# Optimization experiments

Hardware: AMD Instinct MI355X
Metric: run time of the kernel (lower is better)

The kernel has to match this reference:

```python
import jax, jax.numpy as jnp
import numpy as np

SIZE = 128
WIN = SIZE // 4   # sliding-window size == region size (32)
HALF = WIN // 2   # 16


def _conv(x, w, pad, groups=1):
    return jax.lax.conv_general_dilated(x, w, (1, 1), [(pad, pad), (pad, pad)],
        dimension_numbers=('NCHW', 'OIHW', 'NCHW'), feature_group_count=groups)


def _resize(x, h, w):
    # F.interpolate(..., mode='bilinear', align_corners=False)
    return jax.image.resize(x, (x.shape[0], x.shape[1], h, w), 'bilinear', antialias=False)


def _gauss_kernels():
    ax = np.linspace(-2.0, 2.0, 5)
    xx, yy = np.meshgrid(ax, ax)
    g = np.exp(-(xx ** 2 + yy ** 2) / 2.0) / (2.0 * np.pi)  # sigma = 1
    gx = (-xx * g).astype(np.float32)
    gy = (-yy * g).astype(np.float32)
    return (jnp.asarray(np.tile(gx[None, None], (3, 3, 1, 1))),
            jnp.asarray(np.tile(gy[None, None], (3, 3, 1, 1))))


def _edge_extract(x):
    Gx, Gy = _gauss_kernels()
    h = _conv(x, Gx, 2)
    v = _conv(x, Gy, 2)
    return jnp.tanh(jnp.sqrt(h * h + v * v + 1e-8))


def _color_moments(x, win=5):
    # F.unfold-based local mean / unbiased var / skewness, via depthwise box sums
    C = x.shape[1]
    n = float(win * win)
    ones = jnp.ones((C, 1, win, win), x.dtype)
    box = lambda z: _conv(z, ones, win // 2, groups=C)
    s1 = box(x); s2 = box(x * x); s3 = box(x * x * x)
    mean = s1 / n
    var = (s2 - n * mean * mean) / (n - 1.0)               # unbiased, matches torch.var
    m3 = (s3 - 3.0 * mean * s2 + 2.0 * n * mean ** 3) / n  # E[(x-m)^3]
    skew = m3 / (jnp.sqrt(jnp.maximum(var, 0.0)) ** 3 + 1e-6)
    return jnp.concatenate([mean, var, skew], 1)


def _locate_region(c):
    # scipy: gradient magnitude < 0.2 -> 4-connected label at argmax -> bbox center
    H, W = c.shape
    flat = jnp.argmax(c)
    xm = (flat // W).astype(jnp.int32)
    ym = (flat % W).astype(jnp.int32)
    gm = jnp.hypot(jnp.gradient(c, axis=0), jnp.gradient(c, axis=1))
    mask = gm < 0.2
    seed = jnp.zeros((H, W), bool).at[xm, ym].set(True) & mask

    def dil(r):
        d = r
        d = d | jnp.pad(r[1:, :], ((0, 1), (0, 0)))
        d = d | jnp.pad(r[:-1, :], ((1, 0), (0, 0)))
        d = d | jnp.pad(r[:, 1:], ((0, 0), (0, 1)))
        d = d | jnp.pad(r[:, :-1], ((0, 0), (1, 0)))
        return d & mask

    def body(s):
        r, _ = s
        nr = dil(r)
        return (nr, jnp.any(nr != r))

    region, _ = jax.lax.while_loop(lambda s: s[1], body, (seed, jnp.any(seed)))
    rows = jnp.any(region, 1); cols = jnp.any(region, 0)
    rs = jnp.argmax(rows); re = H - jnp.argmax(rows[::-1])
    cs = jnp.argmax(cols); ce = W - jnp.argmax(cols[::-1])
    ok = mask[xm, ym]  # label_at_max != 0
    x1 = jnp.where(ok, ((rs + re) // 2).astype(jnp.int32), xm)
    y1 = jnp.where(ok, ((cs + ce) // 2).astype(jnp.int32), ym)
    return x1, y1


def _affine_grid(move, H, W):
    # theta = [[1,0,tx],[0,1,ty]] with (tx,ty)=move, align_corners=False
    bx = (2.0 * jnp.arange(W, dtype=jnp.float32) + 1.0) / W - 1.0
    by = (2.0 * jnp.arange(H, dtype=jnp.float32) + 1.0) / H - 1.0
    gx = bx[None, None, :] + move[:, 0, None, None]
    gy = by[None, :, None] + move[:, 1, None, None]
    return jnp.stack(jnp.broadcast_arrays(gx, gy), -1)  # [B,H,W,2]


def _grid_sample(x, grid):
    # bilinear, zeros padding, align_corners=False (torch defaults)
    B, C, H, W = x.shape
    ix = ((grid[..., 0] + 1.0) * W - 1.0) / 2.0
    iy = ((grid[..., 1] + 1.0) * H - 1.0) / 2.0
    ix0 = jnp.floor(ix).astype(jnp.int32)
    iy0 = jnp.floor(iy).astype(jnp.int32)
    wx1 = ix - ix0; wy1 = iy - iy0
    b = jnp.arange(B)[:, None, None]

    def g(yy, xx):
        valid = ((xx >= 0) & (xx < W) & (yy >= 0) & (yy < H)).astype(x.dtype)
        v = x[b, :, jnp.clip(yy, 0, H - 1), jnp.clip(xx, 0, W - 1)]  # [B,Hg,Wg,C]
        return v * valid[..., None]

    out = (g(iy0, ix0) * ((1 - wy1) * (1 - wx1))[..., None]
         + g(iy0, ix0 + 1) * ((1 - wy1) * wx1)[..., None]
         + g(iy0 + 1, ix0) * (wy1 * (1 - wx1))[..., None]
         + g(iy0 + 1, ix0 + 1) * (wy1 * wx1)[..., None])
    return jnp.transpose(out, (0, 3, 1, 2))


def _bn_relu6(x, w, b):
    # BatchNorm2d in training mode (batch stats, biased var, eps=1e-5) + ReLU6
    m = x.mean((0, 2, 3), keepdims=True)
    v = ((x - m) ** 2).mean((0, 2, 3), keepdims=True)
    y = (x - m) / jnp.sqrt(v + 1e-5) * w[None, :, None, None] + b[None, :, None, None]
    return jnp.clip(y, 0.0, 6.0)


def setup_inputs():
    key = jax.random.key(0)
    ks = jax.random.split(key, 8)
    B, C = 8, 64
    return dict(
        warm_flag=1,
        feat1=jax.random.normal(ks[0], (B, C, SIZE, SIZE), jnp.float32),
        feat2=jax.random.normal(ks[1], (B, C, SIZE, SIZE), jnp.float32),
        cam1=jax.random.uniform(ks[2], (B, 64, 64), jnp.float32),
        cam2=jax.random.uniform(ks[3], (B, 64, 64), jnp.float32),
        f_g=jax.random.uniform(ks[4], (B, 3, 512, 512), jnp.float32),
        f_e=jax.random.uniform(ks[5], (B, 3, 512, 512), jnp.float32),
        conv1_w=jax.random.normal(ks[6], (C, 3, 3, 3), jnp.float32) * 0.1,
        conv1_b=jnp.zeros((C,), jnp.float32),
        conv2_w=jax.random.normal(ks[7], (C, 9, 3, 3), jnp.float32) * 0.1,
        conv2_b=jnp.zeros((C,), jnp.float32),
        bn_w=jnp.ones((C,), jnp.float32),
        bn_b=jnp.zeros((C,), jnp.float32),
    )


def reference(warm_flag, feat1, feat2, cam1, cam2, f_g, f_e,
              conv1_w, conv1_b, conv2_w, conv2_b, bn_w, bn_b):
    B = cam1.shape[0]
    c1 = _resize(cam1[:, None], SIZE, SIZE)
    c2 = _resize(cam2[:, None], SIZE, SIZE)

    if warm_flag == 1:
        # numpy/scipy path in torch is detached from autograd
        c1s = jax.lax.stop_gradient(c1)
        c2s = jax.lax.stop_gradient(c2)
        x1, y1 = jax.vmap(_locate_region)(c1s[:, 0])
        # valid-mode box convolution of cam2 with ones((H//4, W//4)), argmax
        box = jax.lax.conv_general_dilated(c2s, jnp.ones((1, 1, WIN, WIN), c2.dtype), (1, 1),
            'VALID', dimension_numbers=('NCHW', 'OIHW', 'NCHW'))[:, 0]
        Wv = box.shape[-1]
        flat = jnp.argmax(box.reshape(B, -1), -1)
        x2 = (flat // Wv + HALF).astype(jnp.int32)
        y2 = (flat % Wv + HALF).astype(jnp.int32)

        idx = jnp.arange(SIZE)
        def rect(xc, yc):
            r = (idx[None, :] >= jnp.maximum(xc - HALF, 0)[:, None]) & \
                (idx[None, :] < jnp.minimum(xc + HALF, SIZE)[:, None])
            cc = (idx[None, :] >= jnp.maximum(yc - HALF, 0)[:, None]) & \
                 (idx[None, :] < jnp.minimum(yc + HALF, SIZE)[:, None])
            return r[:, None, :, None] & cc[:, None, None, :]
        mask1 = rect(x1, y1).astype(feat1.dtype)
        mask2 = rect(x2, y2).astype(feat2.dtype)
        mi1 = jnp.stack([x1, y1], -1).astype(jnp.float32)
        mi2 = jnp.stack([x2, y2], -1).astype(jnp.float32)
    else:
        mask1 = jnp.zeros_like(feat1)
        mask2 = jnp.zeros_like(feat2)
        mi1 = jnp.zeros((B, 2), jnp.float32)
        mi2 = jnp.zeros((B, 2), jnp.float32)

    cam2_move = (mi2 - mi1) / (SIZE // 2)
    cam1_move = (mi1 - mi2) / (SIZE // 2)
    grid1 = _affine_grid(cam1_move, SIZE, SIZE)
    grid2 = _affine_grid(cam2_move, SIZE, SIZE)

    moments = _resize(_color_moments(f_e), SIZE, SIZE)   # [B,9,128,128]
    edge = _resize(_edge_extract(f_g), SIZE, SIZE)       # [B,3,128,128]
    feat1_edge = jnp.clip(_conv(edge, conv1_w, 1) + conv1_b[None, :, None, None], 0.0, 6.0)
    feat2_color = _conv(moments, conv2_w, 1) + conv2_b[None, :, None, None]

    feat2_move = _grid_sample(feat2_color * mask2, grid2)
    feat1_edge_move = _grid_sample(feat1_edge * mask1, grid1)

    Bc, C, H, W = feat1.shape
    f1 = feat1.reshape(Bc, C, -1)
    f2 = feat2.reshape(Bc, C, -1)
    f2m = feat2_move.reshape(Bc, C, -1)
    f1m = feat1_edge_move.reshape(Bc, C, -1)

    f2_attn = jax.nn.softmax(jnp.einsum('bcn,bdn->bcd', f2m, f1), -1)  # [B,C,C]
    feat1_apply = jnp.einsum('bcd,bdn->bcn', f2_attn, f1).reshape(Bc, C, H, W)
    f1_attn = jax.nn.softmax(jnp.einsum('bcn,bdn->bcd', f1m, f2), -1)
    feat2_apply = jnp.einsum('bcd,bdn->bcn', f1_attn, f2).reshape(Bc, C, H, W)

    feat1_apply = _bn_relu6(feat1_apply, bn_w, bn_b)
    feat2_apply = _bn_relu6(feat2_apply, bn_w, bn_b)

    if warm_flag == 0:
        return (feat1, feat2, grid1, grid2, feat1_edge, feat2_color, f1_attn, f2_attn, feat1, feat2)
    return (feat1_apply, feat2_apply, grid1, grid2, feat1_edge, feat2_color, f1_attn, f2_attn, feat1, feat2)
```

## Files before the change

### kernel.cpp

```cpp
#include <hip/hip_runtime.h>
#include <math.h>

#define SIZE 128
#define WIN 32
#define HALF 16
#define B 8
#define C 64
#define N (SIZE*SIZE)
#define BCN 8388608
#define BV 97

#define O_APPLY1   0
#define O_APPLY2   8388608
#define O_GRID1    16777216
#define O_GRID2    17039360
#define O_EDGEF    17301504
#define O_COLORF   25690112
#define O_ATTN1    34078720
#define O_ATTN2    34111488
#define O_FEAT1    34144256
#define O_FEAT2    42532864

#define WS_BNP     0
#define WS_XY      361472
#define WS_MOM     361600
#define WS_EDGE    1541248
#define WS_BN      1737856

#define NEGINF (-3.402823466e+38f)

typedef unsigned __int128 u128;

__device__ __forceinline__ u128 hfill(u128 g, u128 m) {
  u128 p = m;
  g |= p & (g << 1);  p &= p << 1;
  g |= p & (g << 2);  p &= p << 2;
  g |= p & (g << 4);  p &= p << 4;
  g |= p & (g << 8);  p &= p << 8;
  g |= p & (g << 16); p &= p << 16;
  g |= p & (g << 32); p &= p << 32;
  g |= p & (g << 64);
  p = m;
  g |= p & (g >> 1);  p &= p >> 1;
  g |= p & (g >> 2);  p &= p >> 2;
  g |= p & (g >> 4);  p &= p >> 4;
  g |= p & (g >> 8);  p &= p >> 8;
  g |= p & (g >> 16); p &= p >> 16;
  g |= p & (g >> 32); p &= p >> 32;
  g |= p & (g >> 64);
  return g;
}

__device__ __forceinline__ float resamp(const float* raw, int i, int j) {
  float fy = fminf(fmaxf(0.5f * (float)i - 0.25f, 0.f), 63.f);
  float fx = fminf(fmaxf(0.5f * (float)j - 0.25f, 0.f), 63.f);
  int y0 = (int)fy; float ty = fy - (float)y0; int y1i = min(y0 + 1, 63);
  int x0 = (int)fx; float tx = fx - (float)x0; int x1i = min(x0 + 1, 63);
  float a00 = raw[y0 * 64 + x0],  a01 = raw[y0 * 64 + x1i];
  float a10 = raw[y1i * 64 + x0], a11 = raw[y1i * 64 + x1i];
  return (1.f - ty) * ((1.f - tx) * a00 + tx * a01)
       + ty * ((1.f - tx) * a10 + tx * a11);
}

#define FRONT_B   8
#define PREP_BASE 16
#define COPY_BASE 2064
#define COPY_HALF 8192
#define STAGE1_GRID (COPY_BASE + 2 * COPY_HALF)

__global__ __launch_bounds__(256) void k_stage1(
    const float* __restrict__ cam1, const float* __restrict__ cam2,
    int* __restrict__ xy,
    const float* __restrict__ fe, const float* __restrict__ fg,
    float* __restrict__ mom, float* __restrict__ edge,
    const float4* __restrict__ f1, float4* __restrict__ o8,
    const float4* __restrict__ f2, float4* __restrict__ o9) {
  __shared__ __align__(16) float smem[33824];
  int blk = blockIdx.x;
  int tid = threadIdx.x;

  if (blk >= COPY_BASE) {
    int c = blk - COPY_BASE;
    if (c < COPY_HALF) o8[c * 256 + tid] = f1[c * 256 + tid];
    else { int i = (c - COPY_HALF) * 256 + tid; o9[i] = f2[i]; }
    return;
  }

  if (blk >= PREP_BASE) {
    float* sx = smem;
    int pblk = blk - PREP_BASE;
    if (pblk < 1536) {
      int tile = pblk & 63, ch = (pblk >> 6) % 3, b = pblk / 192;
      int ti0 = (tile >> 3) * 16, tj0 = (tile & 7) * 16;
      const float* src = fe + (size_t)(b * 3 + ch) * 262144;
      int oy0 = 4 * ti0 - 1, ox0 = 4 * tj0 - 1;
      for (int l = tid; l < 66 * 66; l += 256) {
        int r = l / 66, cc = l % 66;
        int gy = oy0 + r, gx = ox0 + cc;
        sx[l] = (gy >= 0 && gy < 512 && gx >= 0 && gx < 512) ? src[gy * 512 + gx] : 0.f;
      }
      __syncthreads();
      int ii = tid >> 4, jj = tid & 15;
      int i = ti0 + ii, j = tj0 + jj;
      float s1a[6], s2a[6], s3a[6], s1b[6], s2b[6], s3b[6];
      #pragma unroll
      for (int t = 0; t < 6; ++t) {
        float a1 = 0, a2 = 0, a3 = 0, b1 = 0, b2 = 0, b3 = 0;
        int lx = 4 * jj + t;
        #pragma unroll
        for (int r = 0; r < 6; ++r) {
          float v = sx[(4 * ii + r) * 66 + lx];
          float v2 = v * v, v3 = v2 * v;
          if (r < 5) { a1 += v; a2 += v2; a3 += v3; }
          if (r > 0) { b1 += v; b2 += v2; b3 += v3; }
        }
        s1a[t] = a1; s2a[t] = a2; s3a[t] = a3;
        s1b[t] = b1; s2b[t] = b2; s3b[t] = b3;
      }
      float am = 0, av = 0, as = 0;
      #pragma unroll
      for (int py = 0; py < 2; ++py) {
        #pragma unroll
        for (int px = 0; px < 2; ++px) {
          float s1 = 0, s2 = 0, s3 = 0;
          #pragma unroll
          for (int t = 0; t < 5; ++t) {
            s1 += py ? s1b[px + t] : s1a[px + t];
            s2 += py ? s2b[px + t] : s2a[px + t];
            s3 += py ? s3b[px + t] : s3a[px + t];
          }
          float mean = s1 / 25.f;
          float var  = (s2 - 25.f * mean * mean) / 24.f;
          float m3   = (s3 - 3.f * mean * s2 + 50.f * mean * mean * mean) / 25.f;
          float sq   = sqrtf(fmaxf(var, 0.f));
          float skew = m3 / (sq * sq * sq + 1e-6f);
          am += mean; av += var; as += skew;
        }
      }
      int base = (b * 9 + ch) * N + i * 128 + j;
      mom[base]         = 0.25f * am;
      mom[base + 3 * N] = 0.25f * av;
      mom[base + 6 * N] = 0.25f * as;
    } else {
      int eblk = pblk - 1536;
      int tile = eblk & 63, b = eblk >> 6;
      int ti0 = (tile >> 3) * 16, tj0 = (tile & 7) * 16;
      const float* s0 = fg + (size_t)b * 3 * 262144;
      int oy0 = 4 * ti0 - 1, ox0 = 4 * tj0 - 1;
      for (int l = tid; l < 66 * 66; l += 256) {
        int r = l / 66, cc = l % 66;
        int gy = oy0 + r, gx = ox0 + cc;
        float v = 0.f;
        if (gy >= 0 && gy < 512 && gx >= 0 && gx < 512) {
          int o = gy * 512 + gx;
          v = s0[o] + s0[262144 + o] + s0[524288 + o];
        }
        sx[l] = v;
      }
      __syncthreads();
      int ii = tid >> 4, jj = tid & 15;
      int i = ti0 + ii, j = tj0 + jj;
      const float INV2PI = 0.15915494309189535f;
      float wg[5], ug[5];
      #pragma unroll
      for (int t = 0; t < 5; ++t) {
        float a = (float)t - 2.f;
        float e = expf(-0.5f * a * a);
        wg[t] = e; ug[t] = -a * e;
      }
      float rAa[6], rAb[6], rBa[6], rBb[6];
      #pragma unroll
      for (int t = 0; t < 6; ++t) {
        float aa = 0, ab = 0, ba = 0, bb = 0;
        int lx = 4 * jj + t;
        #pragma unroll
        for (int r = 0; r < 6; ++r) {
          float v = sx[(4 * ii + r) * 66 + lx];
          if (r < 5) { aa += v * wg[r]; ba += v * ug[r]; }
          if (r > 0) { ab += v * wg[r - 1]; bb += v * ug[r - 1]; }
        }
        rAa[t] = aa; rAb[t] = ab; rBa[t] = ba; rBb[t] = bb;
      }
      float acc = 0.f;
      #pragma unroll
      for (int py = 0; py < 2; ++py) {
        #pragma unroll
        for (int px = 0; px < 2; ++px) {
          float h = 0, v = 0;
          #pragma unroll
          for (int t = 0; t < 5; ++t) {
            float A  = py ? rAb[px + t] : rAa[px + t];
            float Bw = py ? rBb[px + t] : rBa[px + t];
            h += A * ug[t];
            v += Bw * wg[t];
          }
          h *= INV2PI; v *= INV2PI;
          acc += tanhf(sqrtf(h * h + v * v + 1e-8f));
        }
      }
      edge[b * N + i * 128 + j] = 0.25f * acc;
    }
    return;
  }

  if (blk >= FRONT_B) {
    int b = blk - FRONT_B;
    float* raw = smem;
    float* sc2 = smem + 4096;
    float* cs  = smem + 20480;
    float* sv  = smem + 32896;
    int*   si  = (int*)(smem + 33152);

    const float4* c4 = (const float4*)(cam2 + b * 4096);
    float4* r4 = (float4*)raw;
    #pragma unroll
    for (int k = 0; k < 4; ++k) r4[k * 256 + tid] = c4[k * 256 + tid];
    __syncthreads();
    for (int k = 0; k < 64; ++k) {
      int pix = k * 256 + tid;
      sc2[pix] = resamp(raw, pix >> 7, pix & 127);
    }
    __syncthreads();

    for (int idx = tid; idx < BV * 128; idx += 256) {
      int rr = idx >> 7, cc = idx & 127;
      float acc = 0.f;
      #pragma unroll
      for (int dy = 0; dy < WIN; ++dy) acc += sc2[(rr + dy) * 128 + cc];
      cs[idx] = acc;
    }
    __syncthreads();

    float bv = NEGINF; int bi = 0;
    for (int p = tid; p < BV * BV; p += 256) {
      int rr = p / BV, cc = p % BV;
      float s = 0.f;
      #pragma unroll
      for (int dx = 0; dx < WIN; ++dx) s += cs[rr * 128 + cc + dx];
      if (s > bv) { bv = s; bi = p; }
    }
    sv[tid] = bv; si[tid] = bi;
    __syncthreads();
    for (int s = 128; s; s >>= 1) {
      if (tid < s) {
        float ov = sv[tid + s]; int oi = si[tid + s];
        if (ov > sv[tid] || (ov == sv[tid] && oi < si[tid])) { sv[tid] = ov; si[tid] = oi; }
      }
      __syncthreads();
    }
    if (tid == 0) {
      xy[16 + b] = si[0] / BV + HALF;
      xy[24 + b] = si[0] % BV + HALF;
    }
    return;
  }

  {
    int b = blk;
    float* raw = smem;
    float* sc  = smem + 4096;
    float* sv  = smem + 20480;
    int*   si  = (int*)(smem + 20736);
    unsigned long long* mask64 = (unsigned long long*)(smem + 20992);
    int* sint = (int*)(smem + 21504);

    const float4* c4 = (const float4*)(cam1 + b * 4096);
    float4* r4 = (float4*)raw;
    #pragma unroll
    for (int k = 0; k < 4; ++k) r4[k * 256 + tid] = c4[k * 256 + tid];
    __syncthreads();

    float bv = NEGINF; int bi = 0;
    for (int k = 0; k < 64; ++k) {
      int pix = k * 256 + tid;
      float v1 = resamp(raw, pix >> 7, pix & 127);
      sc[pix] = v1;
      if (v1 > bv) { bv = v1; bi = pix; }
    }
    sv[tid] = bv; si[tid] = bi;
    __syncthreads();
    for (int s = 128; s; s >>= 1) {
      if (tid < s) {
        float ov = sv[tid + s]; int oi = si[tid + s];
        if (ov > sv[tid] || (ov == sv[tid] && oi < si[tid])) { sv[tid] = ov; si[tid] = oi; }
      }
      __syncthreads();
    }
    if (tid == 0) { sint[0] = si[0] >> 7; sint[1] = si[0] & 127; }
    __syncthreads();
    int s_xm = sint[0], s_ym = sint[1];

    for (int k = 0; k < 64; ++k) {
      int pix = k * 256 + tid;
      int i = pix >> 7, j = pix & 127;
      float gx_, gy_;
      if (i == 0)        gx_ = sc[128 + j] - sc[j];
      else if (i == 127) gx_ = sc[127 * 128 + j] - sc[126 * 128 + j];
      else               gx_ = 0.5f * (sc[(i + 1) * 128 + j] - sc[(i - 1) * 128 + j]);
      if (j == 0)        gy_ = sc[i * 128 + 1] - sc[i * 128];
      else if (j == 127) gy_ = sc[i * 128 + 127] - sc[i * 128 + 126];
      else               gy_ = 0.5f * (sc[i * 128 + j + 1] - sc[i * 128 + j - 1]);
      bool pred = hypotf(gx_, gy_) < 0.2f;
      unsigned long long bal = __ballot(pred);
      if ((tid & 63) == 0) mask64[(i << 1) + (j >> 6)] = bal;
    }
    __syncthreads();
    if (tid == 0) {
      unsigned long long wdd = mask64[(s_xm << 1) + (s_ym >> 6)];
      sint[2] = (int)((wdd >> (s_ym & 63)) & 1ull);
    }
    __syncthreads();
    int s_ok = sint[2];

    if (tid < 64) {
      int l = tid;
      u128 m0 = ((u128)mask64[4 * l])     | ((u128)mask64[4 * l + 1] << 64);
      u128 m1 = ((u128)mask64[4 * l + 2]) | ((u128)mask64[4 * l + 3] << 64);
      u128 g0 = 0, g1v = 0;
      if (s_ok && (s_xm >> 1) == l) {
        if ((s_xm & 1) == 0) g0  = ((u128)1) << s_ym;
        else                 g1v = ((u128)1) << s_ym;
      }
      g0  = hfill(g0 & m0, m0);
      g1v = hfill(g1v & m1, m1);
      for (;;) {
        unsigned long long ulo = __shfl_up((unsigned long long)g1v, 1);
        unsigned long long uhi = __shfl_up((unsigned long long)(g1v >> 64), 1);
        u128 up = (l > 0) ? (((u128)ulo) | ((u128)uhi << 64)) : (u128)0;
        unsigned long long dlo = __shfl_down((unsigned long long)g0, 1);
        unsigned long long dhi = __shfl_down((unsigned long long)(g0 >> 64), 1);
        u128 dn = (l < 63) ? (((u128)dlo) | ((u128)dhi << 64)) : (u128)0;
        u128 n0 = hfill((g0 | up | g1v) & m0, m0);
        u128 n1 = hfill((g1v | n0 | dn) & m1, m1);
        bool chg = (n0 != g0) || (n1 != g1v);
        g0 = n0; g1v = n1;
        if (!__any(chg)) break;
      }
      unsigned long long be = __ballot(g0 != 0);
      unsigned long long bo = __ballot(g1v != 0);
      unsigned long long cl = (unsigned long long)(g0 | g1v);
      unsigned long long chh = (unsigned long long)((g0 | g1v) >> 64);
      for (int off = 32; off; off >>= 1) {
        cl  |= __shfl_xor(cl, off);
        chh |= __shfl_xor(chh, off);
      }
      if (l == 0) {
        int rs = 0, re = 0, cs_ = 0, ce = 0;
        if (be | bo) {
          int af = be ? (__ffsll(be) - 1) : 1000;
          int bf = bo ? (__ffsll(bo) - 1) : 1000;
          rs = min(af * 2, bf * 2 + 1);
          int al = be ? (63 - __clzll(be)) : -1000;
          int bl = bo ? (63 - __clzll(bo)) : -1000;
          re = max(al * 2, bl * 2 + 1) + 1;
          cs_ = cl ? (__ffsll(cl) - 1) : 64 + (__ffsll(chh) - 1);
          ce = chh ? 128 - __clzll(chh) : 64 - __clzll(cl);
        }
        int x1, y1;
        if (s_ok) { x1 = (rs + re) >> 1; y1 = (cs_ + ce) >> 1; }
        else      { x1 = s_xm;           y1 = s_ym; }
        xy[b] = x1; xy[8 + b] = y1;
      }
    }
  }
}

__global__ __launch_bounds__(256) void k_conv12(
    const float* __restrict__ edge, const float* __restrict__ w1,
    const float* __restrict__ b1, float* __restrict__ o4,
    const float* __restrict__ mom, const float* __restrict__ w2,
    const float* __restrict__ b2, float* __restrict__ o5,
    const int* __restrict__ xy, float* __restrict__ g1, float* __restrict__ g2) {
  __shared__ float tin[9 * 324];
  __shared__ float wsm[64 * 84];
  int tid = threadIdx.x;

  if (blockIdx.x >= 512) {
    if (blockIdx.y != 0) return;
    int b = blockIdx.x - 512;
    float x1f = (float)xy[b], y1f = (float)xy[8 + b];
    float x2f = (float)xy[16 + b], y2f = (float)xy[24 + b];
    float m1x = (x1f - x2f) / 64.f, m1y = (y1f - y2f) / 64.f;
    float* g1b = g1 + (size_t)b * N * 2;
    float* g2b = g2 + (size_t)b * N * 2;
    for (int k = 0; k < 64; ++k) {
      int pix = k * 256 + tid;
      int h = pix >> 7, w = pix & 127;
      float bx = (2.f * (float)w + 1.f) / 128.f - 1.f;
      float by = (2.f * (float)h + 1.f) / 128.f - 1.f;
      g1b[pix * 2]     = bx + m1x; g1b[pix * 2 + 1] = by + m1y;
      g2b[pix * 2]     = bx - m1x; g2b[pix * 2 + 1] = by - m1y;
    }
    return;
  }

  int b = blockIdx.x >> 6, tile = blockIdx.x & 63;
  int ti0 = (tile >> 3) * 16, tj0 = (tile & 7) * 16;
  int i = tid >> 4, j = tid & 15;
  if (blockIdx.y == 0) {
    for (int l = tid; l < 324; l += 256) {
      int r = l / 18, cc = l % 18;
      int gi = ti0 + r - 1, gj = tj0 + cc - 1;
      tin[l] = (gi >= 0 && gi < 128 && gj >= 0 && gj < 128) ? edge[b * N + gi * 128 + gj] : 0.f;
    }
    for (int l = tid; l < 64 * 12; l += 256) {
      int o = l / 12, t = l % 12;
      wsm[l] = (t < 9) ? (w1[o * 27 + t] + w1[o * 27 + 9 + t] + w1[o * 27 + 18 + t]) : 0.f;
    }
    __syncthreads();
    float win[12];
    #pragma unroll
    for (int dy = 0; dy < 3; ++dy)
      #pragma unroll
      for (int dx = 0; dx < 3; ++dx)
        win[dy * 3 + dx] = tin[(i + dy) * 18 + (j + dx)];
    win[9] = 0.f; win[10] = 0.f; win[11] = 0.f;
    float* o = o4 + (size_t)b * C * N + (ti0 + i) * 128 + tj0 + j;
    for (int oc = 0; oc < C; ++oc) {
      const float4* wr = (const float4*)(wsm + oc * 12);
      float acc = b1[oc];
      #pragma unroll
      for (int q = 0; q < 3; ++q) {
        float4 w4 = wr[q];
        acc += w4.x * win[4 * q] + w4.y * win[4 * q + 1]
             + w4.z * win[4 * q + 2] + w4.w * win[4 * q + 3];
      }
      o[oc * N] = fminf(fmaxf(acc, 0.f), 6.f);
    }
  } else {
    for (int l = tid; l < 9 * 324; l += 256) {
      int ic = l / 324, rem = l % 324, r = rem / 18, cc = rem % 18;
      int gi = ti0 + r - 1, gj = tj0 + cc - 1;
      tin[l] = (gi >= 0 && gi < 128 && gj >= 0 && gj < 128) ? mom[(b * 9 + ic) * N + gi * 128 + gj] : 0.f;
    }
    for (int l = tid; l < 64 * 84; l += 256) {
      int o = l / 84, t = l % 84;
      wsm[l] = (t < 81) ? w2[o * 81 + t] : 0.f;
    }
    __syncthreads();
    float win[84];
    #pragma unroll
    for (int ic = 0; ic < 9; ++ic)
      #pragma unroll
      for (int dy = 0; dy < 3; ++dy)
        #pragma unroll
        for (int dx = 0; dx < 3; ++dx)
          win[ic * 9 + dy * 3 + dx] = tin[ic * 324 + (i + dy) * 18 + (j + dx)];
    win[81] = 0.f; win[82] = 0.f; win[83] = 0.f;
    float* o = o5 + (size_t)b * C * N + (ti0 + i) * 128 + tj0 + j;
    for (int oc = 0; oc < C; ++oc) {
      const float4* wr = (const float4*)(wsm + oc * 84);
      float acc = b2[oc];
      #pragma unroll
      for (int q = 0; q < 21; ++q) {
        float4 w4 = wr[q];
        acc += w4.x * win[4 * q] + w4.y * win[4 * q + 1]
             + w4.z * win[4 * q + 2] + w4.w * win[4 * q + 3];
      }
      o[oc * N] = acc;
    }
  }
}

__global__ __launch_bounds__(256) void k_logits(const float* __restrict__ aB1,
                                                const float* __restrict__ bB1,
                                                const float* __restrict__ aB2,
                                                const float* __restrict__ bB2,
                                                float* __restrict__ lg,
                                                const int* __restrict__ xy) {
  int mode = blockIdx.y;
  const float* aBase = mode ? aB2 : aB1;
  const float* bBase = mode ? bB2 : bB1;
  int b = blockIdx.x >> 4, sl = blockIdx.x & 15;
  int tid = threadIdx.x;
  int ci = (tid >> 4) << 2, di = (tid & 15) << 2;
  float* o = lg + (size_t)(((mode * 8 + b) * 16 + sl)) * 4096;

  int x1 = xy[b], y1 = xy[8 + b], x2 = xy[16 + b], y2 = xy[24 + b];
  int dyh, dxw, rlo, rhi, clo, chi;
  if (mode == 0) {
    dyh = y1 - y2; dxw = x1 - x2;
    rlo = max(x1 - HALF, 0); rhi = min(x1 + HALF, SIZE);
    clo = max(y1 - HALF, 0); chi = min(y1 + HALF, SIZE);
  } else {
    dyh = y2 - y1; dxw = x2 - x1;
    rlo = max(x2 - HALF, 0); rhi = min(x2 + HALF, SIZE);
    clo = max(y2 - HALF, 0); chi = min(y2 + HALF, SIZE);
  }
  int hlo = max(0, rlo - dyh), hhi = min(SIZE, rhi - dyh);
  int wlo = max(0, clo - dxw), whi = min(SIZE, chi - dxw);
  int wn = whi - wlo, hn = hhi - hlo;
  int npos = (wn > 0 && hn > 0) ? wn * hn : 0;
  if (sl * 64 >= npos) {
    #pragma unroll
    for (int u = 0; u < 4; ++u)
      #pragma unroll
      for (int v = 0; v < 4; ++v)
        o[(ci + u) * 64 + (di + v)] = 0.f;
    return;
  }

  __shared__ float aS[64][65];
  __shared__ float bS[64][65];
  const float* aB = aBase + (size_t)b * C * N;
  const float* bB = bBase + (size_t)b * C * N;
  for (int l = tid; l < 4096; l += 256) {
    int ch = l >> 6, k = l & 63;
    int p = sl * 64 + k;
    float av = 0.f, bv = 0.f;
    if (p < npos) {
      int h = hlo + p / wn, w = wlo + p % wn;
      av = aB[ch * N + (h + dyh) * 128 + (w + dxw)];
      bv = bB[ch * N + h * 128 + w];
    }
    aS[ch][k] = av; bS[ch][k] = bv;
  }
  __syncthreads();
  float acc[4][4] = {};
  #pragma unroll 4
  for (int k = 0; k < 64; ++k) {
    float a0 = aS[ci][k], a1 = aS[ci + 1][k], a2 = aS[ci + 2][k], a3 = aS[ci + 3][k];
    float b0 = bS[di][k], b1v = bS[di + 1][k], b2v = bS[di + 2][k], b3 = bS[di + 3][k];
    acc[0][0] += a0 * b0; acc[0][1] += a0 * b1v; acc[0][2] += a0 * b2v; acc[0][3] += a0 * b3;
    acc[1][0] += a1 * b0; acc[1][1] += a1 * b1v; acc[1][2] += a1 * b2v; acc[1][3] += a1 * b3;
    acc[2][0] += a2 * b0; acc[2][1] += a2 * b1v; acc[2][2] += a2 * b2v; acc[2][3] += a2 * b3;
    acc[3][0] += a3 * b0; acc[3][1] += a3 * b1v; acc[3][2] += a3 * b2v; acc[3][3] += a3 * b3;
  }
  #pragma unroll
  for (int u = 0; u < 4; ++u)
    #pragma unroll
    for (int v = 0; v < 4; ++v)
      o[(ci + u) * 64 + (di + v)] = acc[u][v];
}

__global__ void k_softmax(const float* __restrict__ lg,
                          float* __restrict__ o6, float* __restrict__ o7) {
  int row = blockIdx.x;
  int mode = blockIdx.y;
  float* dst = mode ? o7 : o6;
  int b = row >> 6, c = row & 63;
  int lane = threadIdx.x;
  const float* base = lg + (size_t)((mode * 8 + b) * 16) * 4096 + c * 64 + lane;
  float v = 0.f;
  #pragma unroll
  for (int sl = 0; sl < 16; ++sl) v += base[sl * 4096];
  float mx = v;
  for (int off = 32; off; off >>= 1) mx = fmaxf(mx, __shfl_xor(mx, off));
  float e = expf(v - mx);
  float s = e;
  for (int off = 32; off; off >>= 1) s += __shfl_xor(s, off);
  dst[row * 64 + lane] = e / s;
}

__global__ __launch_bounds__(256) void k_applyst(const float* __restrict__ a1,
                                                 const float* __restrict__ s1_,
                                                 float* __restrict__ d1,
                                                 const float* __restrict__ a2,
                                                 const float* __restrict__ s2_,
                                                 float* __restrict__ d2,
                                                 float* __restrict__ bnp) {
  const float* attn; const float* src; float* dst;
  int t = blockIdx.y;
  if (t == 0) { attn = a1; src = s1_; dst = d1; }
  else        { attn = a2; src = s2_; dst = d2; }
  int b = blockIdx.x >> 6, chunk = blockIdx.x & 63;
  int n0 = chunk * 256 + threadIdx.x;
  const float* s = src + (size_t)b * C * N + n0;
  float v[64];
  #pragma unroll
  for (int d = 0; d < 64; ++d) v[d] = s[d * N];
  const float4* at4 = (const float4*)(attn + b * 4096);
  float* o = dst + (size_t)b * C * N + n0;
  __shared__ float red[64][4], red2[64][4];
  int lane = threadIdx.x & 63, wave = threadIdx.x >> 6;
  for (int c = 0; c < 64; ++c) {
    float acc = 0.f;
    #pragma unroll
    for (int q = 0; q < 16; ++q) {
      float4 w4 = at4[c * 16 + q];
      acc += w4.x * v[4 * q] + w4.y * v[4 * q + 1] + w4.z * v[4 * q + 2] + w4.w * v[4 * q + 3];
    }
    o[c * N] = acc;
    float sr = acc, ssr = acc * acc;
    for (int off = 32; off; off >>= 1) {
      sr  += __shfl_xor(sr, off);
      ssr += __shfl_xor(ssr, off);
    }
    if (lane == 0) { red[c][wave] = sr; red2[c][wave] = ssr; }
  }
  __syncthreads();
  if (threadIdx.x < 64) {
    int c = threadIdx.x;
    float sr  = red[c][0] + red[c][1] + red[c][2] + red[c][3];
    float ssr = red2[c][0] + red2[c][1] + red2[c][2] + red2[c][3];
    int idx = (t * 64 + c) * 512 + blockIdx.x;
    bnp[idx]         = sr;
    bnp[65536 + idx] = ssr;
  }
}

__global__ void k_bnstats2(const float* __restrict__ bnp, float* __restrict__ stats) {
  __shared__ float sr[128][4], ssr[128][4];
  int tid = threadIdx.x;
  int combo = tid >> 2, q = tid & 3;
  float s = 0.f, ss = 0.f;
  for (int k = 0; k < 128; ++k) {
    int idx = combo * 512 + q * 128 + k;
    s  += bnp[idx];
    ss += bnp[65536 + idx];
  }
  sr[combo][q] = s; ssr[combo][q] = ss;
  __syncthreads();
  if (q == 0) {
    float S  = sr[combo][0] + sr[combo][1] + sr[combo][2] + sr[combo][3];
    float SS = ssr[combo][0] + ssr[combo][1] + ssr[combo][2] + ssr[combo][3];
    int t = combo >> 6, c = combo & 63;
    float mean = S / 131072.f;
    float var  = SS / 131072.f - mean * mean;
    stats[t * 128 + c]      = mean;
    stats[t * 128 + 64 + c] = 1.f / sqrtf(var + 1e-5f);
  }
}

__global__ __launch_bounds__(256) void k_bnapply(
    float4* __restrict__ o0, float4* __restrict__ o1,
    const float* __restrict__ stats,
    const float* __restrict__ bw, const float* __restrict__ bb) {
  int i = blockIdx.x * 256 + threadIdx.x;
  int t = blockIdx.y;
  float4* p = t ? o1 : o0;
  int c = (i >> 12) & 63;
  float m = stats[t * 128 + c], r = stats[t * 128 + 64 + c];
  float w_ = bw[c], b_ = bb[c];
  float4 v = p[i];
  v.x = fminf(fmaxf((v.x - m) * r * w_ + b_, 0.f), 6.f);
  v.y = fminf(fmaxf((v.y - m) * r * w_ + b_, 0.f), 6.f);
  v.z = fminf(fmaxf((v.z - m) * r * w_ + b_, 0.f), 6.f);
  v.w = fminf(fmaxf((v.w - m) * r * w_ + b_, 0.f), 6.f);
  p[i] = v;
}

extern "C" void kernel_launch(void* const* d_in, const int* in_sizes, int n_in,
                              void* d_out, int out_size, void* d_ws, size_t ws_size,
                              hipStream_t stream) {
  const float* feat1   = (const float*)d_in[1];
  const float* feat2   = (const float*)d_in[2];
  const float* cam1    = (const float*)d_in[3];
  const float* cam2    = (const float*)d_in[4];
  const float* f_g     = (const float*)d_in[5];
  const float* f_e     = (const float*)d_in[6];
  const float* conv1_w = (const float*)d_in[7];
  const float* conv1_b = (const float*)d_in[8];
  const float* conv2_w = (const float*)d_in[9];
  const float* conv2_b = (const float*)d_in[10];
  const float* bn_w    = (const float*)d_in[11];
  const float* bn_b    = (const float*)d_in[12];

  float* out = (float*)d_out;
  float* w = (float*)d_ws;
  int* xy = (int*)(w + WS_XY);

  float* o0 = out + O_APPLY1;
  float* o1 = out + O_APPLY2;
  float* o2 = out + O_GRID1;
  float* o3 = out + O_GRID2;
  float* o4 = out + O_EDGEF;
  float* o5 = out + O_COLORF;
  float* o6 = out + O_ATTN1;
  float* o7 = out + O_ATTN2;
  float* o8 = out + O_FEAT1;
  float* o9 = out + O_FEAT2;

  k_stage1<<<STAGE1_GRID, 256, 0, stream>>>(
      cam1, cam2, xy,
      f_e, f_g, w + WS_MOM, w + WS_EDGE,
      (const float4*)feat1, (float4*)o8, (const float4*)feat2, (float4*)o9);

  k_conv12<<<dim3(520, 2), 256, 0, stream>>>(w + WS_EDGE, conv1_w, conv1_b, o4,
                                             w + WS_MOM, conv2_w, conv2_b, o5,
                                             xy, o2, o3);

  k_logits<<<dim3(B * 16, 2), 256, 0, stream>>>(o4, feat2, o5, feat1,
                                                w + WS_MOM, xy);

  k_softmax<<<dim3(B * C, 2), 64, 0, stream>>>(w + WS_MOM, o6, o7);

  k_applyst<<<dim3(B * 64, 2), 256, 0, stream>>>(o7, feat1, o0, o6, feat2, o1,
                                                 w + WS_BNP);

  k_bnstats2<<<1, 512, 0, stream>>>(w + WS_BNP, w + WS_BN);

  k_bnapply<<<dim3(BCN / 4 / 256, 2), 256, 0, stream>>>(
      (float4*)o0, (float4*)o1, w + WS_BN, bn_w, bn_b);
}
```

Measured before the change: 587.7 us.

## Shrink stage1 shared memory by recomputing resampled maps and widen copy blocks

```diff
diff --git a/kernel.cpp b/kernel.cpp
--- a/kernel.cpp
+++ b/kernel.cpp
@@ -65,24 +65,42 @@
 #define FRONT_B   8
 #define PREP_BASE 16
 #define COPY_BASE 2064
-#define COPY_HALF 8192
-#define STAGE1_GRID (COPY_BASE + 2 * COPY_HALF)
-
-__global__ __launch_bounds__(256) void k_stage1(
+#define COPY_BLKS 1024
+#define STAGE1_GRID (COPY_BASE + 2 * COPY_BLKS)
+
+__global__ __launch_bounds__(256, 4) void k_stage1(
     const float* __restrict__ cam1, const float* __restrict__ cam2,
     int* __restrict__ xy,
     const float* __restrict__ fe, const float* __restrict__ fg,
     float* __restrict__ mom, float* __restrict__ edge,
     const float4* __restrict__ f1, float4* __restrict__ o8,
     const float4* __restrict__ f2, float4* __restrict__ o9) {
-  __shared__ __align__(16) float smem[33824];
+  __shared__ __align__(16) float smem[5632];
   int blk = blockIdx.x;
   int tid = threadIdx.x;
 
   if (blk >= COPY_BASE) {
     int c = blk - COPY_BASE;
-    if (c < COPY_HALF) o8[c * 256 + tid] = f1[c * 256 + tid];
-    else { int i = (c - COPY_HALF) * 256 + tid; o9[i] = f2[i]; }
+    const float4* s; float4* d;
+    if (c < COPY_BLKS) { s = f1; d = o8; }
+    else               { s = f2; d = o9; c -= COPY_BLKS; }
+    int base = c * 2048 + tid;
+    float4 v0 = s[base];
+    float4 v1 = s[base + 256];
+    float4 v2 = s[base + 512];
+    float4 v3 = s[base + 768];
+    float4 v4 = s[base + 1024];
+    float4 v5 = s[base + 1280];
+    float4 v6 = s[base + 1536];
+    float4 v7 = s[base + 1792];
+    d[base]        = v0;
+    d[base + 256]  = v1;
+    d[base + 512]  = v2;
+    d[base + 768]  = v3;
+    d[base + 1024] = v4;
+    d[base + 1280] = v5;
+    d[base + 1536] = v6;
+    d[base + 1792] = v7;
     return;
   }
 
@@ -206,38 +224,34 @@
   if (blk >= FRONT_B) {
     int b = blk - FRONT_B;
     float* raw = smem;
-    float* sc2 = smem + 4096;
-    float* cs  = smem + 20480;
-    float* sv  = smem + 32896;
-    int*   si  = (int*)(smem + 33152);
+    float* buf = smem + 4096;
+    float* sv  = smem + 5120;
+    int*   si  = (int*)(smem + 5376);
 
     const float4* c4 = (const float4*)(cam2 + b * 4096);
     float4* r4 = (float4*)raw;
     #pragma unroll
     for (int k = 0; k < 4; ++k) r4[k * 256 + tid] = c4[k * 256 + tid];
     __syncthreads();
-    for (int k = 0; k < 64; ++k) {
-      int pix = k * 256 + tid;
-      sc2[pix] = resamp(raw, pix >> 7, pix & 127);
-    }
-    __syncthreads();
-
-    for (int idx = tid; idx < BV * 128; idx += 256) {
-      int rr = idx >> 7, cc = idx & 127;
-      float acc = 0.f;
-      #pragma unroll
-      for (int dy = 0; dy < WIN; ++dy) acc += sc2[(rr + dy) * 128 + cc];
-      cs[idx] = acc;
-    }
-    __syncthreads();
 
     float bv = NEGINF; int bi = 0;
-    for (int p = tid; p < BV * BV; p += 256) {
-      int rr = p / BV, cc = p % BV;
-      float s = 0.f;
-      #pragma unroll
-      for (int dx = 0; dx < WIN; ++dx) s += cs[rr * 128 + cc + dx];
-      if (s > bv) { bv = s; bi = p; }
+    for (int r0 = 0; r0 < BV; r0 += 8) {
+      int nr = min(8, BV - r0);
+      for (int idx = tid; idx < nr * 128; idx += 256) {
+        int rr = r0 + (idx >> 7), cc = idx & 127;
+        float acc = 0.f;
+        for (int dy = 0; dy < WIN; ++dy) acc += resamp(raw, rr + dy, cc);
+        buf[idx] = acc;
+      }
+      __syncthreads();
+      for (int q = tid; q < nr * BV; q += 256) {
+        int rr = q / BV, cc = q % BV;
+        float s = 0.f;
+        #pragma unroll
+        for (int dx = 0; dx < WIN; ++dx) s += buf[rr * 128 + cc + dx];
+        if (s > bv) { bv = s; bi = (r0 + rr) * BV + cc; }
+      }
+      __syncthreads();
     }
     sv[tid] = bv; si[tid] = bi;
     __syncthreads();
@@ -258,11 +272,10 @@
   {
     int b = blk;
     float* raw = smem;
-    float* sc  = smem + 4096;
-    float* sv  = smem + 20480;
-    int*   si  = (int*)(smem + 20736);
-    unsigned long long* mask64 = (unsigned long long*)(smem + 20992);
-    int* sint = (int*)(smem + 21504);
+    float* sv  = smem + 4096;
+    int*   si  = (int*)(smem + 4352);
+    unsigned long long* mask64 = (unsigned long long*)(smem + 4608);
+    int* sint = (int*)(smem + 5120);
 
     const float4* c4 = (const float4*)(cam1 + b * 4096);
     float4* r4 = (float4*)raw;
@@ -274,7 +287,6 @@
     for (int k = 0; k < 64; ++k) {
       int pix = k * 256 + tid;
       float v1 = resamp(raw, pix >> 7, pix & 127);
-      sc[pix] = v1;
       if (v1 > bv) { bv = v1; bi = pix; }
     }
     sv[tid] = bv; si[tid] = bi;
@@ -294,12 +306,12 @@
       int pix = k * 256 + tid;
       int i = pix >> 7, j = pix & 127;
       float gx_, gy_;
-      if (i == 0)        gx_ = sc[128 + j] - sc[j];
-      else if (i == 127) gx_ = sc[127 * 128 + j] - sc[126 * 128 + j];
-      else               gx_ = 0.5f * (sc[(i + 1) * 128 + j] - sc[(i - 1) * 128 + j]);
-      if (j == 0)        gy_ = sc[i * 128 + 1] - sc[i * 128];
-      else if (j == 127) gy_ = sc[i * 128 + 127] - sc[i * 128 + 126];
-      else               gy_ = 0.5f * (sc[i * 128 + j + 1] - sc[i * 128 + j - 1]);
+      if (i == 0)        gx_ = resamp(raw, 1, j) - resamp(raw, 0, j);
+      else if (i == 127) gx_ = resamp(raw, 127, j) - resamp(raw, 126, j);
+      else               gx_ = 0.5f * (resamp(raw, i + 1, j) - resamp(raw, i - 1, j));
+      if (j == 0)        gy_ = resamp(raw, i, 1) - resamp(raw, i, 0);
+      else if (j == 127) gy_ = resamp(raw, i, 127) - resamp(raw, i, 126);
+      else               gy_ = 0.5f * (resamp(raw, i, j + 1) - resamp(raw, i, j - 1));
       bool pred = hypotf(gx_, gy_) < 0.2f;
       unsigned long long bal = __ballot(pred);
       if ((tid & 63) == 0) mask64[(i << 1) + (j >> 6)] = bal;
```

Measured after the change: 536.0 us. 8.8% less time.
